# Performance work log

Measured on AMD Instinct MI355X. Metric: run time of the kernel, lower is better.

## Reference

```python
import math
import jax, jax.numpy as jnp
import numpy as np

L, C, FC, K, H, WIN, T, B = 6, 512, 2048, 3, 8, 4, 1024, 4
KC = C // H
EPS = 1e-4


def setup_inputs() -> dict:
    key = jax.random.key(0)
    ks = jax.random.split(key, 20)
    s = 0.05
    f = jnp.float32
    inp = {
        "x": jax.random.normal(ks[0], (B, C, T), f),
        "wq": jax.random.normal(ks[1], (L, C, C), f) * s,
        "bq": jnp.zeros((L, C), f),
        "wk": jax.random.normal(ks[2], (L, C, C), f) * s,
        "bk": jnp.zeros((L, C), f),
        "wv": jax.random.normal(ks[3], (L, C, C), f) * s,
        "bv": jnp.zeros((L, C), f),
        "wo": jax.random.normal(ks[4], (L, C, C), f) * s,
        "bo": jnp.zeros((L, C), f),
        "rel_k": jax.random.normal(ks[5], (L, 1, 2 * WIN + 1, KC), f) * (KC ** -0.5),
        "g1": jnp.ones((L, C), f),
        "be1": jnp.zeros((L, C), f),
        "w1": jax.random.normal(ks[6], (L, FC, C, K), f) * s,
        "bb1": jnp.zeros((L, FC), f),
        "w2": jax.random.normal(ks[7], (L, C, FC, K), f) * s,
        "bb2": jnp.zeros((L, C), f),
        "g2": jnp.ones((L, C), f),
        "be2": jnp.zeros((L, C), f),
    }
    return inp


def conv1d(x, w, b, pad):
    # x: [B,Cin,T], w: [Cout,Cin,K]
    y = jax.lax.conv_general_dilated(x, w, (1,), [(pad, pad)],
                                     dimension_numbers=("NCH", "OIH", "NCH"))
    return y + b[None, :, None]


def layer_norm(x, g, b):
    # normalize over channel dim (axis 1), matching the torch LayerNorm above
    m = jnp.mean(x, 1, keepdims=True)
    v = jnp.mean((x - m) ** 2, 1, keepdims=True)
    return (x - m) * jax.lax.rsqrt(v + EPS) * g[None, :, None] + b[None, :, None]


def get_relative_embeddings(rel, length):
    pad_len = max(length - (WIN + 1), 0)
    start = max(WIN + 1 - length, 0)
    if pad_len > 0:
        rel = jnp.pad(rel, ((0, 0), (pad_len, pad_len), (0, 0)), mode="edge")
    return rel[:, start:start + 2 * length - 1]


def rel_to_abs(x):
    # x: [b,h,l,2l-1] -> [b,h,l,l]  (Music-Transformer skew)
    b, h, l, _ = x.shape
    x = jnp.pad(x, ((0, 0), (0, 0), (0, 0), (0, 1)))          # [b,h,l,2l]
    x = x.reshape(b, h, l * 2 * l)
    x = jnp.pad(x, ((0, 0), (0, 0), (0, l - 1)))
    x = x.reshape(b, h, l + 1, 2 * l - 1)[:, :, :l, l - 1:]
    return x


def attention(x, wq, bq, wk, bk, wv, bv, wo, bo, rel_k):
    b, c, t = x.shape
    q = conv1d(x, wq[:, :, None], bq, 0).reshape(b, H, KC, t)
    k = conv1d(x, wk[:, :, None], bk, 0).reshape(b, H, KC, t)
    v = conv1d(x, wv[:, :, None], bv, 0).reshape(b, H, KC, t)
    scale = 1.0 / math.sqrt(KC)
    scores = jnp.einsum("bhdt,bhds->bhts", q, k) * scale      # [b,H,t,t]
    rel = get_relative_embeddings(rel_k, t)[0]                # [2t-1, KC] (heads_share)
    rel_logits = jnp.einsum("bhdt,md->bhtm", q * scale, rel)  # [b,H,t,2t-1]
    scores = scores + rel_to_abs(rel_logits)
    p = jax.nn.softmax(scores, axis=-1)
    out = jnp.einsum("bhts,bhds->bhdt", p, v).reshape(b, c, t)
    return conv1d(out, wo[:, :, None], bo, 0)


def reference(x, wq, bq, wk, bk, wv, bv, wo, bo, rel_k,
              g1, be1, w1, bb1, w2, bb2, g2, be2):
    for i in range(L):
        y = attention(x, wq[i], bq[i], wk[i], bk[i], wv[i], bv[i],
                      wo[i], bo[i], rel_k[i])
        x = layer_norm(x + y, g1[i], be1[i])
        y = conv1d(jax.nn.relu(conv1d(x, w1[i], bb1[i], K // 2)), w2[i], bb2[i], K // 2)
        x = layer_norm(x + y, g2[i], be2[i])
    return x
```

## Files before the change

kernel.cpp:

```cpp
#include <hip/hip_runtime.h>

constexpr int L  = 6;
constexpr int C  = 512;
constexpr int FC = 2048;
constexpr int H  = 8;
constexpr int KC = 64;
constexpr int T  = 1024;
constexpr int B  = 4;
#define SCALE 0.125f

typedef __bf16 bf16_t;
typedef __bf16 bf16x8 __attribute__((ext_vector_type(8)));
typedef float  f32x4  __attribute__((ext_vector_type(4)));

constexpr size_t OFF_XF    = 0;
constexpr size_t OFF_YF    = OFF_XF   + (size_t)B*T*C*4;
constexpr size_t OFF_XPAD  = OFF_YF   + (size_t)B*T*C*4;
constexpr size_t OFF_Q     = OFF_XPAD + (size_t)B*(T+2)*C*2;
constexpr size_t OFF_K     = OFF_Q    + (size_t)B*T*C*2;
constexpr size_t OFF_VT    = OFF_K    + (size_t)B*T*C*2;
constexpr size_t OFF_YA    = OFF_VT   + (size_t)B*T*C*2;
constexpr size_t OFF_MID   = OFF_YA   + (size_t)B*T*C*2;
constexpr size_t OFF_WQKVO = OFF_MID  + (size_t)B*(T+2)*FC*2;
constexpr size_t OFF_W1    = OFF_WQKVO+ (size_t)4*C*C*2;
constexpr size_t OFF_W2    = OFF_W1   + (size_t)3*FC*C*2;

__device__ __forceinline__ void gload_lds16(const bf16_t* g, bf16_t* l) {
    __builtin_amdgcn_global_load_lds((const __attribute__((address_space(1))) void*)g,
                                     (__attribute__((address_space(3))) void*)l, 16, 0, 0);
}

__global__ __launch_bounds__(256) void cvt4_kernel(const float* __restrict__ a,
                                                   const float* __restrict__ b,
                                                   const float* __restrict__ c,
                                                   const float* __restrict__ d,
                                                   bf16_t* __restrict__ out) {
    int i = blockIdx.x * 256 + threadIdx.x;
    int which = i >> 18;
    int idx   = i & ((1 << 18) - 1);
    const float* s = (which == 0) ? a : (which == 1) ? b : (which == 2) ? c : d;
    out[i] = (bf16_t)s[idx];
}

__global__ __launch_bounds__(256) void cvtw1_kernel(const float* __restrict__ w1, bf16_t* __restrict__ out) {
    int i = blockIdx.x * 256 + threadIdx.x;
    int j = i >> 20;
    int rem = i & ((1 << 20) - 1);
    int fc = rem >> 9, c = rem & 511;
    out[i] = (bf16_t)w1[fc * (C * 3) + c * 3 + j];
}

__global__ __launch_bounds__(256) void cvtw2_kernel(const float* __restrict__ w2, bf16_t* __restrict__ out) {
    int i = blockIdx.x * 256 + threadIdx.x;
    int j = i >> 20;
    int rem = i & ((1 << 20) - 1);
    int c = rem >> 11, fc = rem & 2047;
    out[i] = (bf16_t)w2[c * (FC * 3) + fc * 3 + j];
}

__global__ __launch_bounds__(256) void transpose_in(const float* __restrict__ x0,
                                                    float* __restrict__ xf,
                                                    bf16_t* __restrict__ xpad) {
    __shared__ float tile[32][33];
    int b = blockIdx.z, t0 = blockIdx.x * 32, c0 = blockIdx.y * 32;
    int tx = threadIdx.x, ty = threadIdx.y;
#pragma unroll
    for (int j = 0; j < 4; ++j)
        tile[ty + j * 8][tx] = x0[((size_t)b * C + c0 + ty + j * 8) * T + t0 + tx];
    __syncthreads();
#pragma unroll
    for (int j = 0; j < 4; ++j) {
        float v = tile[tx][ty + j * 8];
        long t = t0 + ty + j * 8;
        xf[((size_t)b * T + t) * C + c0 + tx] = v;
        xpad[((size_t)b * (T + 2) + t + 1) * C + c0 + tx] = (bf16_t)v;
    }
}

__global__ __launch_bounds__(256) void transpose_out(const float* __restrict__ xf,
                                                     float* __restrict__ out) {
    __shared__ float tile[32][33];
    int b = blockIdx.z, t0 = blockIdx.x * 32, c0 = blockIdx.y * 32;
    int tx = threadIdx.x, ty = threadIdx.y;
#pragma unroll
    for (int j = 0; j < 4; ++j)
        tile[ty + j * 8][tx] = xf[((size_t)b * T + t0 + ty + j * 8) * C + c0 + tx];
    __syncthreads();
#pragma unroll
    for (int j = 0; j < 4; ++j)
        out[((size_t)b * C + c0 + ty + j * 8) * T + t0 + tx] = tile[tx][ty + j * 8];
}

__global__ __launch_bounds__(256) void zero_pads(bf16_t* __restrict__ xpad, bf16_t* __restrict__ midp) {
    int i = blockIdx.x * 256 + threadIdx.x;
    if (i < 4096) {
        int b = i >> 10, r = (i >> 9) & 1, c = i & 511;
        xpad[((size_t)b * (T + 2) + (size_t)r * (T + 1)) * C + c] = (bf16_t)0.f;
    } else {
        int j = i - 4096;
        int b = j >> 12, r = (j >> 11) & 1, c = j & 2047;
        midp[((size_t)b * (T + 2) + (size_t)r * (T + 1)) * FC + c] = (bf16_t)0.f;
    }
}

template <int NP>
__global__ __launch_bounds__(256) void add_ln(float* __restrict__ x,
                                              const float* __restrict__ p0, const float* __restrict__ p1,
                                              const float* __restrict__ p2,
                                              const float* __restrict__ g, const float* __restrict__ be,
                                              bf16_t* __restrict__ xpad) {
    long bt = blockIdx.x;
    int tid = threadIdx.x;
    float* xr = x + bt * C;
    float v0 = xr[tid] + p0[bt * C + tid] + p1[bt * C + tid];
    float v1 = xr[tid + 256] + p0[bt * C + tid + 256] + p1[bt * C + tid + 256];
    if (NP == 3) { v0 += p2[bt * C + tid]; v1 += p2[bt * C + tid + 256]; }
    float s = v0 + v1, q = v0 * v0 + v1 * v1;
#pragma unroll
    for (int m = 1; m < 64; m <<= 1) { s += __shfl_xor(s, m); q += __shfl_xor(q, m); }
    __shared__ float ss[4], qq[4];
    int wid = tid >> 6;
    if ((tid & 63) == 0) { ss[wid] = s; qq[wid] = q; }
    __syncthreads();
    s = ss[0] + ss[1] + ss[2] + ss[3];
    q = qq[0] + qq[1] + qq[2] + qq[3];
    float mean = s * (1.f / C);
    float var = q * (1.f / C) - mean * mean;
    float rstd = rsqrtf(var + 1e-4f);
    float o0 = (v0 - mean) * rstd * g[tid] + be[tid];
    float o1 = (v1 - mean) * rstd * g[tid + 256] + be[tid + 256];
    xr[tid] = o0; xr[tid + 256] = o1;
    long b = bt >> 10, t = bt & (T - 1);
    bf16_t* xp = xpad + (b * (T + 2) + t + 1) * C;
    xp[tid] = (bf16_t)o0; xp[tid + 256] = (bf16_t)o1;
}

template <int OUTMODE, bool RELU, int NSPLIT, int IPT, int NTAPS>
__global__ __launch_bounds__(256) void gemm128(
    const bf16_t* __restrict__ A, long batchStrideA, int lda,
    const bf16_t* __restrict__ Bw, long tapStrideB, int ldb,
    const float* __restrict__ bias0, const float* __restrict__ bias1,
    const float* __restrict__ bias2,
    void* __restrict__ Dp, void* __restrict__ D1p, void* __restrict__ D2p,
    long batchStrideD, int ldd) {
    __shared__ bf16_t As[128 * 64];
    __shared__ bf16_t Bs[128 * 64];
    const int tid = threadIdx.x;
    const int lane = tid & 63, wid = tid >> 6;
    const int l15 = lane & 15, quad = lane >> 4;
    const int wy = wid >> 1, wx = wid & 1;
    const int nb = gridDim.z / NSPLIT;
    const int split = (NSPLIT > 1) ? ((int)blockIdx.z / nb) : 0;
    const int b = (int)blockIdx.z - split * nb;

    const bf16_t* Ab = A + (long)b * batchStrideA + (long)blockIdx.y * 128 * lda;
    const bf16_t* Bb = Bw + (long)blockIdx.x * 128 * ldb;

    const int lrow = lane >> 3;
    const int lcolsw = ((lane & 7) ^ lrow) * 8;

    f32x4 acc[4][4];
#pragma unroll
    for (int i = 0; i < 4; ++i)
#pragma unroll
        for (int j = 0; j < 4; ++j) acc[i][j] = (f32x4){0.f, 0.f, 0.f, 0.f};

    constexpr int itersAll = IPT * NTAPS;
    constexpr int per = itersAll / NSPLIT;
    const int it0 = split * per;

    for (int it = it0; it < it0 + per; ++it) {
        const int tap = (NTAPS == 1) ? 0 : (it / IPT);
        const int k0 = (it - tap * IPT) * 64;
        const bf16_t* At = Ab + (long)tap * lda + k0;
        const bf16_t* Bt = Bb + (long)tap * tapStrideB + k0;
        __syncthreads();
#pragma unroll
        for (int i = 0; i < 4; ++i) {
            int chunk = wid * 4 + i;
            int row = chunk * 8 + lrow;
            gload_lds16(At + (long)row * lda + lcolsw, As + chunk * 512 + lane * 8);
            gload_lds16(Bt + (long)row * ldb + lcolsw, Bs + chunk * 512 + lane * 8);
        }
        __syncthreads();
#pragma unroll
        for (int ks = 0; ks < 2; ++ks) {
            bf16x8 bfr[4], afr[4];
#pragma unroll
            for (int nt = 0; nt < 4; ++nt) {
                int row = wx * 64 + nt * 16 + l15;
                bfr[nt] = *(const bf16x8*)&Bs[row * 64 + (((ks * 4 + quad) ^ (l15 & 7)) * 8)];
            }
#pragma unroll
            for (int mt = 0; mt < 4; ++mt) {
                int row = wy * 64 + mt * 16 + l15;
                afr[mt] = *(const bf16x8*)&As[row * 64 + (((ks * 4 + quad) ^ (l15 & 7)) * 8)];
            }
#pragma unroll
            for (int mt = 0; mt < 4; ++mt)
#pragma unroll
                for (int nt = 0; nt < 4; ++nt)
                    acc[mt][nt] = __builtin_amdgcn_mfma_f32_16x16x32_bf16(afr[mt], bfr[nt], acc[mt][nt], 0, 0, 0);
        }
    }

    const long m0 = (long)blockIdx.y * 128 + wy * 64;
    const int n0g = (int)blockIdx.x * 128 + wx * 64;
#pragma unroll
    for (int mt = 0; mt < 4; ++mt) {
        long rowb = m0 + mt * 16 + quad * 4;
#pragma unroll
        for (int nt = 0; nt < 4; ++nt) {
            int col = n0g + nt * 16 + l15;
            if (OUTMODE == 0) {
                float bb = (split == 0) ? bias0[col] : 0.f;
                float* D = ((split == 0) ? (float*)Dp : (split == 1) ? (float*)D1p : (float*)D2p)
                           + (long)b * batchStrideD;
#pragma unroll
                for (int r = 0; r < 4; ++r) D[(rowb + r) * ldd + col] = acc[mt][nt][r] + bb;
            } else if (OUTMODE == 1) {
                float bb = bias0[col];
                bf16_t* D = (bf16_t*)Dp + (long)b * batchStrideD;
#pragma unroll
                for (int r = 0; r < 4; ++r) {
                    float v = acc[mt][nt][r] + bb;
                    if (RELU) v = fmaxf(v, 0.f);
                    D[(rowb + r) * ldd + col] = (bf16_t)v;
                }
            } else {
                int which = col >> 9, cl = col & 511;
                const float* bp = (which == 0) ? bias0 : (which == 1) ? bias1 : bias2;
                float bb = bp[cl];
                if (which < 2) {
                    bf16_t* D = (bf16_t*)((which == 0) ? Dp : D1p) + (long)b * T * C;
#pragma unroll
                    for (int r = 0; r < 4; ++r) D[(rowb + r) * C + cl] = (bf16_t)(acc[mt][nt][r] + bb);
                } else {
                    bf16_t* D = (bf16_t*)D2p + (long)b * C * T;
                    union { bf16_t h[4]; uint2 u; } pk;
#pragma unroll
                    for (int r = 0; r < 4; ++r) pk.h[r] = (bf16_t)(acc[mt][nt][r] + bb);
                    *(uint2*)(D + (long)cl * T + rowb) = pk.u;
                }
            }
        }
    }
}

__global__ __launch_bounds__(256) void attn_kernel(const bf16_t* __restrict__ q,
                                                   const bf16_t* __restrict__ k,
                                                   const bf16_t* __restrict__ vT,
                                                   const float* __restrict__ relk,
                                                   bf16_t* __restrict__ y) {
    const int b = blockIdx.z, h = blockIdx.y;
    const int qt0 = blockIdx.x * 128;
    __shared__ bf16_t qp[128][72];
    __shared__ bf16_t kt[64][72];
    __shared__ bf16_t vt[64][72];
    __shared__ float  rl[128][12];

    const int tid = threadIdx.x;
    const int lane = tid & 63, wid = tid >> 6;
    const int l15 = lane & 15, quad = lane >> 4;

    const bf16_t* qbase = q + ((size_t)(b * T + qt0)) * C + h * 64;
#pragma unroll
    for (int i = 0; i < 4; ++i) {
        int idx = tid + i * 256;
        int r = idx >> 3, c = idx & 7;
        *(uint4*)&qp[r][c * 8] = *(const uint4*)(qbase + (long)r * C + c * 8);
    }
    __syncthreads();

    for (int i = tid; i < 128 * 9; i += 256) {
        int r = i / 9, j = i - r * 9;
        float acc = 0.f;
#pragma unroll
        for (int d = 0; d < 64; ++d) acc += (float)qp[r][d] * relk[j * 64 + d];
        rl[r][j] = acc * SCALE;
    }

    bf16x8 af[2][2];
#pragma unroll
    for (int mt = 0; mt < 2; ++mt)
#pragma unroll
        for (int ks = 0; ks < 2; ++ks)
            af[mt][ks] = *(const bf16x8*)&qp[wid * 32 + mt * 16 + l15][ks * 32 + quad * 8];

    float m_i[2][4], l_i[2][4];
    f32x4 o[2][4];
#pragma unroll
    for (int mt = 0; mt < 2; ++mt)
#pragma unroll
        for (int r = 0; r < 4; ++r) { m_i[mt][r] = -1e30f; l_i[mt][r] = 0.f; }
#pragma unroll
    for (int mt = 0; mt < 2; ++mt)
#pragma unroll
        for (int dn = 0; dn < 4; ++dn) o[mt][dn] = (f32x4){0.f, 0.f, 0.f, 0.f};

    for (int st = 0; st < T / 64; ++st) {
        __syncthreads();
        const bf16_t* kb = k + ((size_t)(b * T + st * 64)) * C + h * 64;
        const bf16_t* vb = vT + ((size_t)(b * C + h * 64)) * T + st * 64;
#pragma unroll
        for (int i = 0; i < 2; ++i) {
            int idx = tid + i * 256;
            int r = idx >> 3, c = idx & 7;
            *(uint4*)&kt[r][c * 8] = *(const uint4*)(kb + (long)r * C + c * 8);
        }
#pragma unroll
        for (int i = 0; i < 2; ++i) {
            int idx = tid + i * 256;
            int r = idx >> 3, c = idx & 7;
            *(uint4*)&vt[r][c * 8] = *(const uint4*)(vb + (long)r * T + c * 8);
        }
        __syncthreads();

        f32x4 sc4[2][4];
#pragma unroll
        for (int mt = 0; mt < 2; ++mt)
#pragma unroll
            for (int nt = 0; nt < 4; ++nt) {
                f32x4 a = (f32x4){0.f, 0.f, 0.f, 0.f};
#pragma unroll
                for (int ks = 0; ks < 2; ++ks) {
                    bf16x8 bfr = *(const bf16x8*)&kt[nt * 16 + l15][ks * 32 + quad * 8];
                    a = __builtin_amdgcn_mfma_f32_16x16x32_bf16(af[mt][ks], bfr, a, 0, 0, 0);
                }
                sc4[mt][nt] = a;
            }

#pragma unroll
        for (int mt = 0; mt < 2; ++mt)
#pragma unroll
            for (int nt = 0; nt < 4; ++nt)
#pragma unroll
                for (int r = 0; r < 4; ++r) {
                    int row = wid * 32 + mt * 16 + quad * 4 + r;
                    int tpos = qt0 + row;
                    int spos = st * 64 + nt * 16 + l15;
                    int j = spos - tpos + 4;
                    j = j < 0 ? 0 : (j > 8 ? 8 : j);
                    sc4[mt][nt][r] = sc4[mt][nt][r] * SCALE + rl[row][j];
                }

        float alpha[2][4];
#pragma unroll
        for (int mt = 0; mt < 2; ++mt)
#pragma unroll
            for (int r = 0; r < 4; ++r) {
                float mx = fmaxf(fmaxf(sc4[mt][0][r], sc4[mt][1][r]), fmaxf(sc4[mt][2][r], sc4[mt][3][r]));
#pragma unroll
                for (int d = 1; d < 16; d <<= 1) mx = fmaxf(mx, __shfl_xor(mx, d));
                float mn = fmaxf(m_i[mt][r], mx);
                alpha[mt][r] = __expf(m_i[mt][r] - mn);
                m_i[mt][r] = mn;
            }
#pragma unroll
        for (int mt = 0; mt < 2; ++mt)
#pragma unroll
            for (int r = 0; r < 4; ++r) {
                float rs = 0.f;
#pragma unroll
                for (int nt = 0; nt < 4; ++nt) {
                    float p = __expf(sc4[mt][nt][r] - m_i[mt][r]);
                    sc4[mt][nt][r] = p;
                    rs += p;
                }
#pragma unroll
                for (int d = 1; d < 16; d <<= 1) rs += __shfl_xor(rs, d);
                l_i[mt][r] = l_i[mt][r] * alpha[mt][r] + rs;
            }
#pragma unroll
        for (int mt = 0; mt < 2; ++mt)
#pragma unroll
            for (int dn = 0; dn < 4; ++dn)
#pragma unroll
                for (int r = 0; r < 4; ++r) o[mt][dn][r] *= alpha[mt][r];

#pragma unroll
        for (int mt = 0; mt < 2; ++mt)
#pragma unroll
            for (int nt = 0; nt < 4; ++nt)
#pragma unroll
                for (int r = 0; r < 4; ++r)
                    qp[wid * 32 + mt * 16 + quad * 4 + r][nt * 16 + l15] = (bf16_t)sc4[mt][nt][r];

#pragma unroll
        for (int mt = 0; mt < 2; ++mt) {
            bf16x8 pa[2];
#pragma unroll
            for (int ks = 0; ks < 2; ++ks)
                pa[ks] = *(const bf16x8*)&qp[wid * 32 + mt * 16 + l15][ks * 32 + quad * 8];
#pragma unroll
            for (int dn = 0; dn < 4; ++dn)
#pragma unroll
                for (int ks = 0; ks < 2; ++ks) {
                    bf16x8 vf = *(const bf16x8*)&vt[dn * 16 + l15][ks * 32 + quad * 8];
                    o[mt][dn] = __builtin_amdgcn_mfma_f32_16x16x32_bf16(pa[ks], vf, o[mt][dn], 0, 0, 0);
                }
        }
    }

    bf16_t* yb = y + ((size_t)(b * T + qt0)) * C + h * 64;
#pragma unroll
    for (int mt = 0; mt < 2; ++mt)
#pragma unroll
        for (int r = 0; r < 4; ++r) {
            float linv = 1.f / l_i[mt][r];
            int row = wid * 32 + mt * 16 + quad * 4 + r;
#pragma unroll
            for (int dn = 0; dn < 4; ++dn)
                yb[(long)row * C + dn * 16 + l15] = (bf16_t)(o[mt][dn][r] * linv);
        }
}

extern "C" void kernel_launch(void* const* d_in, const int* in_sizes, int n_in,
                              void* d_out, int out_size, void* d_ws, size_t ws_size,
                              hipStream_t stream) {
    const float* x0  = (const float*)d_in[0];
    const float* wq  = (const float*)d_in[1];
    const float* bq  = (const float*)d_in[2];
    const float* wk  = (const float*)d_in[3];
    const float* bk  = (const float*)d_in[4];
    const float* wv  = (const float*)d_in[5];
    const float* bv  = (const float*)d_in[6];
    const float* wo  = (const float*)d_in[7];
    const float* bo  = (const float*)d_in[8];
    const float* rlk = (const float*)d_in[9];
    const float* g1  = (const float*)d_in[10];
    const float* be1 = (const float*)d_in[11];
    const float* w1  = (const float*)d_in[12];
    const float* bb1 = (const float*)d_in[13];
    const float* w2  = (const float*)d_in[14];
    const float* bb2 = (const float*)d_in[15];
    const float* g2  = (const float*)d_in[16];
    const float* be2 = (const float*)d_in[17];

    char* ws = (char*)d_ws;
    float*  xf    = (float*)(ws + OFF_XF);
    float*  yf    = (float*)(ws + OFF_YF);
    float*  yf2   = (float*)(ws + OFF_Q);
    float*  yf3   = (float*)(ws + OFF_VT);
    bf16_t* xpad  = (bf16_t*)(ws + OFF_XPAD);
    bf16_t* qb    = (bf16_t*)(ws + OFF_Q);
    bf16_t* kb    = (bf16_t*)(ws + OFF_K);
    bf16_t* vTb   = (bf16_t*)(ws + OFF_VT);
    bf16_t* yab   = (bf16_t*)(ws + OFF_YA);
    bf16_t* midp  = (bf16_t*)(ws + OFF_MID);
    bf16_t* wqkvo = (bf16_t*)(ws + OFF_WQKVO);
    bf16_t* w1b   = (bf16_t*)(ws + OFF_W1);
    bf16_t* w2b   = (bf16_t*)(ws + OFF_W2);

    transpose_in<<<dim3(T / 32, C / 32, B), dim3(32, 8), 0, stream>>>(x0, xf, xpad);
    zero_pads<<<80, 256, 0, stream>>>(xpad, midp);

    for (int l = 0; l < L; ++l) {
        cvt4_kernel<<<4 * C * C / 256, 256, 0, stream>>>(wq + (size_t)l * C * C, wk + (size_t)l * C * C,
                                                         wv + (size_t)l * C * C, wo + (size_t)l * C * C, wqkvo);
        cvtw1_kernel<<<3 * FC * C / 256, 256, 0, stream>>>(w1 + (size_t)l * FC * C * 3, w1b);
        cvtw2_kernel<<<3 * C * FC / 256, 256, 0, stream>>>(w2 + (size_t)l * C * FC * 3, w2b);

        gemm128<3, false, 1, 8, 1><<<dim3(1536 / 128, T / 128, B), 256, 0, stream>>>(
            xpad + C, (long)(T + 2) * C, C, wqkvo, 0, C,
            bq + l * C, bk + l * C, bv + l * C,
            (void*)qb, (void*)kb, (void*)vTb, 0, 0);

        attn_kernel<<<dim3(T / 128, H, B), 256, 0, stream>>>(qb, kb, vTb, rlk + (size_t)l * 9 * KC, yab);

        gemm128<0, false, 2, 8, 1><<<dim3(C / 128, T / 128, 2 * B), 256, 0, stream>>>(
            yab, (long)T * C, C, wqkvo + 3 * C * C, 0, C,
            bo + l * C, nullptr, nullptr,
            (void*)yf, (void*)yf2, nullptr, (long)T * C, C);

        add_ln<2><<<B * T, 256, 0, stream>>>(xf, yf, yf2, nullptr, g1 + l * C, be1 + l * C, xpad);

        gemm128<1, true, 1, 8, 3><<<dim3(FC / 128, T / 128, B), 256, 0, stream>>>(
            xpad, (long)(T + 2) * C, C, w1b, (long)FC * C, C,
            bb1 + l * FC, nullptr, nullptr,
            (void*)(midp + FC), nullptr, nullptr, (long)(T + 2) * FC, FC);

        gemm128<0, false, 3, 32, 3><<<dim3(C / 128, T / 128, 3 * B), 256, 0, stream>>>(
            midp, (long)(T + 2) * FC, FC, w2b, (long)C * FC, FC,
            bb2 + l * C, nullptr, nullptr,
            (void*)yf, (void*)yf2, (void*)yf3, (long)T * C, C);

        add_ln<3><<<B * T, 256, 0, stream>>>(xf, yf, yf2, yf3, g2 + l * C, be2 + l * C, xpad);
    }

    transpose_out<<<dim3(T / 32, C / 32, B), dim3(32, 8), 0, stream>>>(xf, (float*)d_out);
}
```

Baseline: 1.314 ms.

## Double-buffer K/V with async LDS loads, halve attention query tile

The attention kernel now handles 64 query rows per block instead of 128, which doubles the grid to 512 blocks. K and V tiles are double-buffered and prefetched with direct global-to-LDS loads into an XOR-swizzled layout, so the next tile's loads overlap the current tile's MFMA and softmax work and one barrier per step is removed. The softmax folds log2(e) into the scale and relative logits and uses exp2f. In exchange, each block reloads K/V for fewer query rows, roughly doubling K/V global traffic. The Q buffer is reused for P with a different stride, which relies on barrier ordering.

```diff
diff --git a/kernel.cpp b/kernel.cpp
--- a/kernel.cpp
+++ b/kernel.cpp
@@ -8,6 +8,7 @@
 constexpr int T  = 1024;
 constexpr int B  = 4;
 #define SCALE 0.125f
+#define LOG2E 1.4426950408889634f
 
 typedef __bf16 bf16_t;
 typedef __bf16 bf16x8 __attribute__((ext_vector_type(8)));
@@ -253,166 +254,152 @@
                                                    const float* __restrict__ relk,
                                                    bf16_t* __restrict__ y) {
     const int b = blockIdx.z, h = blockIdx.y;
-    const int qt0 = blockIdx.x * 128;
-    __shared__ bf16_t qp[128][72];
-    __shared__ bf16_t kt[64][72];
-    __shared__ bf16_t vt[64][72];
-    __shared__ float  rl[128][12];
+    const int qt0 = blockIdx.x * 64;
+    __shared__ bf16_t qps[64 * 72];
+    __shared__ bf16_t ktb[2][64 * 64];
+    __shared__ bf16_t vtb[2][64 * 64];
+    __shared__ float  rl[64][12];
 
     const int tid = threadIdx.x;
     const int lane = tid & 63, wid = tid >> 6;
     const int l15 = lane & 15, quad = lane >> 4;
+    const int lrow = lane >> 3;
+    const int su   = ((lane & 7) ^ lrow) * 8;
 
     const bf16_t* qbase = q + ((size_t)(b * T + qt0)) * C + h * 64;
-#pragma unroll
-    for (int i = 0; i < 4; ++i) {
-        int idx = tid + i * 256;
-        int r = idx >> 3, c = idx & 7;
-        *(uint4*)&qp[r][c * 8] = *(const uint4*)(qbase + (long)r * C + c * 8);
+    const bf16_t* kbs = k + ((size_t)(b * T)) * C + h * 64;
+    const bf16_t* vbs = vT + ((size_t)(b * C + h * 64)) * T;
+#pragma unroll
+    for (int i = 0; i < 2; ++i) {
+        int chunk = wid * 2 + i;
+        int row = chunk * 8 + lrow;
+        gload_lds16(qbase + (long)row * C + su, qps + chunk * 512 + lane * 8);
+        gload_lds16(kbs + (long)row * C + su, ktb[0] + chunk * 512 + lane * 8);
+        gload_lds16(vbs + (long)row * T + su, vtb[0] + chunk * 512 + lane * 8);
     }
     __syncthreads();
 
-    for (int i = tid; i < 128 * 9; i += 256) {
+    for (int i = tid; i < 64 * 9; i += 256) {
         int r = i / 9, j = i - r * 9;
         float acc = 0.f;
 #pragma unroll
-        for (int d = 0; d < 64; ++d) acc += (float)qp[r][d] * relk[j * 64 + d];
-        rl[r][j] = acc * SCALE;
-    }
-
-    bf16x8 af[2][2];
-#pragma unroll
-    for (int mt = 0; mt < 2; ++mt)
-#pragma unroll
-        for (int ks = 0; ks < 2; ++ks)
-            af[mt][ks] = *(const bf16x8*)&qp[wid * 32 + mt * 16 + l15][ks * 32 + quad * 8];
-
-    float m_i[2][4], l_i[2][4];
-    f32x4 o[2][4];
-#pragma unroll
-    for (int mt = 0; mt < 2; ++mt)
-#pragma unroll
-        for (int r = 0; r < 4; ++r) { m_i[mt][r] = -1e30f; l_i[mt][r] = 0.f; }
-#pragma unroll
-    for (int mt = 0; mt < 2; ++mt)
-#pragma unroll
-        for (int dn = 0; dn < 4; ++dn) o[mt][dn] = (f32x4){0.f, 0.f, 0.f, 0.f};
+        for (int d = 0; d < 64; ++d)
+            acc += (float)qps[r * 64 + ((d >> 3) ^ (r & 7)) * 8 + (d & 7)] * relk[j * 64 + d];
+        rl[r][j] = acc * (SCALE * LOG2E);
+    }
+
+    bf16x8 af[2];
+#pragma unroll
+    for (int ks = 0; ks < 2; ++ks) {
+        int r = wid * 16 + l15;
+        af[ks] = *(const bf16x8*)&qps[r * 64 + (((ks * 4 + quad) ^ (r & 7)) * 8)];
+    }
+
+    float m_i[4], l_i[4];
+    f32x4 o[4];
+#pragma unroll
+    for (int r = 0; r < 4; ++r) { m_i[r] = -1e30f; l_i[r] = 0.f; }
+#pragma unroll
+    for (int dn = 0; dn < 4; ++dn) o[dn] = (f32x4){0.f, 0.f, 0.f, 0.f};
 
     for (int st = 0; st < T / 64; ++st) {
         __syncthreads();
-        const bf16_t* kb = k + ((size_t)(b * T + st * 64)) * C + h * 64;
-        const bf16_t* vb = vT + ((size_t)(b * C + h * 64)) * T + st * 64;
-#pragma unroll
-        for (int i = 0; i < 2; ++i) {
-            int idx = tid + i * 256;
-            int r = idx >> 3, c = idx & 7;
-            *(uint4*)&kt[r][c * 8] = *(const uint4*)(kb + (long)r * C + c * 8);
-        }
-#pragma unroll
-        for (int i = 0; i < 2; ++i) {
-            int idx = tid + i * 256;
-            int r = idx >> 3, c = idx & 7;
-            *(uint4*)&vt[r][c * 8] = *(const uint4*)(vb + (long)r * T + c * 8);
-        }
-        __syncthreads();
-
-        f32x4 sc4[2][4];
-#pragma unroll
-        for (int mt = 0; mt < 2; ++mt)
+        if (st < T / 64 - 1) {
+            const bf16_t* kb = kbs + (size_t)(st + 1) * 64 * C;
+            const bf16_t* vb = vbs + (st + 1) * 64;
+            bf16_t* kd = ktb[(st + 1) & 1];
+            bf16_t* vd = vtb[(st + 1) & 1];
+#pragma unroll
+            for (int i = 0; i < 2; ++i) {
+                int chunk = wid * 2 + i;
+                int row = chunk * 8 + lrow;
+                gload_lds16(kb + (long)row * C + su, kd + chunk * 512 + lane * 8);
+                gload_lds16(vb + (long)row * T + su, vd + chunk * 512 + lane * 8);
+            }
+        }
+        const bf16_t* ktc = ktb[st & 1];
+        const bf16_t* vtc = vtb[st & 1];
+
+        f32x4 sc[4];
+#pragma unroll
+        for (int nt = 0; nt < 4; ++nt) {
+            f32x4 a = (f32x4){0.f, 0.f, 0.f, 0.f};
+#pragma unroll
+            for (int ks = 0; ks < 2; ++ks) {
+                int rr = nt * 16 + l15;
+                bf16x8 bfr = *(const bf16x8*)&ktc[rr * 64 + (((ks * 4 + quad) ^ (l15 & 7)) * 8)];
+                a = __builtin_amdgcn_mfma_f32_16x16x32_bf16(af[ks], bfr, a, 0, 0, 0);
+            }
+            sc[nt] = a;
+        }
+
+#pragma unroll
+        for (int nt = 0; nt < 4; ++nt)
+#pragma unroll
+            for (int r = 0; r < 4; ++r) {
+                int row = wid * 16 + quad * 4 + r;
+                int j = (st * 64 + nt * 16 + l15) - (qt0 + row) + 4;
+                j = j < 0 ? 0 : (j > 8 ? 8 : j);
+                sc[nt][r] = sc[nt][r] * (SCALE * LOG2E) + rl[row][j];
+            }
+
+        float alpha[4];
+#pragma unroll
+        for (int r = 0; r < 4; ++r) {
+            float mx = fmaxf(fmaxf(sc[0][r], sc[1][r]), fmaxf(sc[2][r], sc[3][r]));
+#pragma unroll
+            for (int d = 1; d < 16; d <<= 1) mx = fmaxf(mx, __shfl_xor(mx, d));
+            float mn = fmaxf(m_i[r], mx);
+            alpha[r] = exp2f(m_i[r] - mn);
+            m_i[r] = mn;
+        }
+#pragma unroll
+        for (int r = 0; r < 4; ++r) {
+            float rs = 0.f;
 #pragma unroll
             for (int nt = 0; nt < 4; ++nt) {
-                f32x4 a = (f32x4){0.f, 0.f, 0.f, 0.f};
-#pragma unroll
-                for (int ks = 0; ks < 2; ++ks) {
-                    bf16x8 bfr = *(const bf16x8*)&kt[nt * 16 + l15][ks * 32 + quad * 8];
-                    a = __builtin_amdgcn_mfma_f32_16x16x32_bf16(af[mt][ks], bfr, a, 0, 0, 0);
-                }
-                sc4[mt][nt] = a;
-            }
-
-#pragma unroll
-        for (int mt = 0; mt < 2; ++mt)
-#pragma unroll
-            for (int nt = 0; nt < 4; ++nt)
-#pragma unroll
-                for (int r = 0; r < 4; ++r) {
-                    int row = wid * 32 + mt * 16 + quad * 4 + r;
-                    int tpos = qt0 + row;
-                    int spos = st * 64 + nt * 16 + l15;
-                    int j = spos - tpos + 4;
-                    j = j < 0 ? 0 : (j > 8 ? 8 : j);
-                    sc4[mt][nt][r] = sc4[mt][nt][r] * SCALE + rl[row][j];
-                }
-
-        float alpha[2][4];
-#pragma unroll
-        for (int mt = 0; mt < 2; ++mt)
-#pragma unroll
-            for (int r = 0; r < 4; ++r) {
-                float mx = fmaxf(fmaxf(sc4[mt][0][r], sc4[mt][1][r]), fmaxf(sc4[mt][2][r], sc4[mt][3][r]));
-#pragma unroll
-                for (int d = 1; d < 16; d <<= 1) mx = fmaxf(mx, __shfl_xor(mx, d));
-                float mn = fmaxf(m_i[mt][r], mx);
-                alpha[mt][r] = __expf(m_i[mt][r] - mn);
-                m_i[mt][r] = mn;
-            }
-#pragma unroll
-        for (int mt = 0; mt < 2; ++mt)
-#pragma unroll
-            for (int r = 0; r < 4; ++r) {
-                float rs = 0.f;
-#pragma unroll
-                for (int nt = 0; nt < 4; ++nt) {
-                    float p = __expf(sc4[mt][nt][r] - m_i[mt][r]);
-                    sc4[mt][nt][r] = p;
-                    rs += p;
-                }
-#pragma unroll
-                for (int d = 1; d < 16; d <<= 1) rs += __shfl_xor(rs, d);
-                l_i[mt][r] = l_i[mt][r] * alpha[mt][r] + rs;
-            }
-#pragma unroll
-        for (int mt = 0; mt < 2; ++mt)
-#pragma unroll
-            for (int dn = 0; dn < 4; ++dn)
-#pragma unroll
-                for (int r = 0; r < 4; ++r) o[mt][dn][r] *= alpha[mt][r];
-
-#pragma unroll
-        for (int mt = 0; mt < 2; ++mt)
-#pragma unroll
-            for (int nt = 0; nt < 4; ++nt)
-#pragma unroll
-                for (int r = 0; r < 4; ++r)
-                    qp[wid * 32 + mt * 16 + quad * 4 + r][nt * 16 + l15] = (bf16_t)sc4[mt][nt][r];
-
-#pragma unroll
-        for (int mt = 0; mt < 2; ++mt) {
-            bf16x8 pa[2];
-#pragma unroll
-            for (int ks = 0; ks < 2; ++ks)
-                pa[ks] = *(const bf16x8*)&qp[wid * 32 + mt * 16 + l15][ks * 32 + quad * 8];
-#pragma unroll
-            for (int dn = 0; dn < 4; ++dn)
-#pragma unroll
-                for (int ks = 0; ks < 2; ++ks) {
-                    bf16x8 vf = *(const bf16x8*)&vt[dn * 16 + l15][ks * 32 + quad * 8];
-                    o[mt][dn] = __builtin_amdgcn_mfma_f32_16x16x32_bf16(pa[ks], vf, o[mt][dn], 0, 0, 0);
-                }
-        }
+                float p = exp2f(sc[nt][r] - m_i[r]);
+                sc[nt][r] = p;
+                rs += p;
+            }
+#pragma unroll
+            for (int d = 1; d < 16; d <<= 1) rs += __shfl_xor(rs, d);
+            l_i[r] = l_i[r] * alpha[r] + rs;
+        }
+#pragma unroll
+        for (int dn = 0; dn < 4; ++dn)
+#pragma unroll
+            for (int r = 0; r < 4; ++r) o[dn][r] *= alpha[r];
+
+#pragma unroll
+        for (int nt = 0; nt < 4; ++nt)
+#pragma unroll
+            for (int r = 0; r < 4; ++r)
+                qps[(wid * 16 + quad * 4 + r) * 72 + nt * 16 + l15] = (bf16_t)sc[nt][r];
+
+        bf16x8 pa[2];
+#pragma unroll
+        for (int ks = 0; ks < 2; ++ks)
+            pa[ks] = *(const bf16x8*)&qps[(wid * 16 + l15) * 72 + ks * 32 + quad * 8];
+#pragma unroll
+        for (int dn = 0; dn < 4; ++dn)
+#pragma unroll
+            for (int ks = 0; ks < 2; ++ks) {
+                int rr = dn * 16 + l15;
+                bf16x8 vf = *(const bf16x8*)&vtc[rr * 64 + (((ks * 4 + quad) ^ (l15 & 7)) * 8)];
+                o[dn] = __builtin_amdgcn_mfma_f32_16x16x32_bf16(pa[ks], vf, o[dn], 0, 0, 0);
+            }
     }
 
     bf16_t* yb = y + ((size_t)(b * T + qt0)) * C + h * 64;
 #pragma unroll
-    for (int mt = 0; mt < 2; ++mt)
-#pragma unroll
-        for (int r = 0; r < 4; ++r) {
-            float linv = 1.f / l_i[mt][r];
-            int row = wid * 32 + mt * 16 + quad * 4 + r;
-#pragma unroll
-            for (int dn = 0; dn < 4; ++dn)
-                yb[(long)row * C + dn * 16 + l15] = (bf16_t)(o[mt][dn][r] * linv);
-        }
+    for (int r = 0; r < 4; ++r) {
+        float linv = 1.f / l_i[r];
+        int row = wid * 16 + quad * 4 + r;
+#pragma unroll
+        for (int dn = 0; dn < 4; ++dn)
+            yb[(long)row * C + dn * 16 + l15] = (bf16_t)(o[dn][r] * linv);
+    }
 }
 
 extern "C" void kernel_launch(void* const* d_in, const int* in_sizes, int n_in,
@@ -466,7 +453,7 @@
             bq + l * C, bk + l * C, bv + l * C,
             (void*)qb, (void*)kb, (void*)vTb, 0, 0);
 
-        attn_kernel<<<dim3(T / 128, H, B), 256, 0, stream>>>(qb, kb, vTb, rlk + (size_t)l * 9 * KC, yab);
+        attn_kernel<<<dim3(T / 64, H, B), 256, 0, stream>>>(qb, kb, vTb, rlk + (size_t)l * 9 * KC, yab);
 
         gemm128<0, false, 2, 8, 1><<<dim3(C / 128, T / 128, 2 * B), 256, 0, stream>>>(
             yab, (long)T * C, C, wqkvo + 3 * C * C, 0, C,
```

Result: no change. 1.306 ms (-0.6%).
